# Performance work log

Hardware: AMD Instinct MI355X
Metric: run time of the kernel (lower is better)

Reference implementation:

```python
import math
import jax, jax.numpy as jnp
import numpy as np

B, S, H = 8, 1024, 1024
NH = 16
HD = H // NH  # 64


def setup_inputs() -> dict:
    key = jax.random.key(0)
    k1, k2, k3, k4 = jax.random.split(key, 4)
    hidden_states = jax.random.normal(k1, (B, S, H), dtype=jnp.float32)
    attention_mask = jax.random.randint(k2, (B, 1, 1, S), 0, 2, dtype=jnp.int32)
    w_qkv = jax.random.normal(k3, (H, 3 * H), dtype=jnp.float32) * (1.0 / math.sqrt(H))
    b_qkv = jax.random.normal(k4, (3 * H,), dtype=jnp.float32) * 0.02
    return {"hidden_states": hidden_states, "attention_mask": attention_mask,
            "w_qkv": w_qkv, "b_qkv": b_qkv}


def reference(hidden_states, attention_mask, w_qkv, b_qkv):
    b, s, _ = hidden_states.shape
    # fused QKV projection: [b, s, 3H]
    qkv = jnp.einsum('bsh,hk->bsk', hidden_states, w_qkv) + b_qkv
    # view (b, s, nh, 3*hd) -> permute -> chunk last dim (per-head q|k|v layout)
    qkv = qkv.reshape(b, s, NH, 3, HD)
    qkv = jnp.transpose(qkv, (0, 2, 1, 3, 4))      # [b, nh, s, 3, hd]
    q, k, v = qkv[..., 0, :], qkv[..., 1, :], qkv[..., 2, :]
    # raw scores, then FusedScaleMaskSoftmax semantics: scale * scores, mask, fp32 softmax
    scores = jnp.einsum('bhqd,bhkd->bhqk', q, k)
    scale = math.sqrt(HD)  # module passes sqrt(head_dim) as multiplicative scale
    scores = scores.astype(jnp.float32) * scale
    mask = attention_mask != 0                     # nonzero -> masked (padding)
    scores = jnp.where(mask, jnp.float32(-10000.0), scores)
    probs = jax.nn.softmax(scores, axis=-1).astype(hidden_states.dtype)
    # dropout prob = 0 -> identity
    context = jnp.einsum('bhqk,bhkd->bhqd', probs, v)
    context = jnp.transpose(context, (0, 2, 1, 3)).reshape(b, s, NH * HD)
    return context
```

## Files before the change

kernel.cpp:

```cpp
#include <hip/hip_runtime.h>
#include <math.h>

#define Bdim 8
#define Sdim 1024
#define Hdim 1024
#define NHd 16
#define HDd 64
#define N3H 3072

#define Q_OFF   0u
#define K_OFF   16777216u
#define V_OFF   33554432u
#define WH_OFF  41943040u
#define WL_OFF  45088768u
#define AHI_OFF 0u
#define ALO_OFF 8388608u

typedef __bf16 bf16x8 __attribute__((ext_vector_type(8)));
typedef float  f32x4  __attribute__((ext_vector_type(4)));

__device__ __forceinline__ unsigned short f2bf(float x) {
  unsigned b = __builtin_bit_cast(unsigned, x);
  return (unsigned short)((b + 0x7FFFu + ((b >> 16) & 1u)) >> 16);
}
__device__ __forceinline__ float bf2f(unsigned short h) {
  unsigned b = ((unsigned)h) << 16;
  return __builtin_bit_cast(float, b);
}
__device__ __forceinline__ void split_hl(float v, unsigned short& h, unsigned short& l) {
  h = f2bf(v);
  l = f2bf(v - bf2f(h));
}
__device__ __forceinline__ void async16(void* lds, const void* g) {
  __builtin_amdgcn_global_load_lds((const __attribute__((address_space(1))) unsigned int*)g,
                                   (__attribute__((address_space(3))) unsigned int*)lds, 16, 0, 0);
}

__global__ __launch_bounds__(256) void convert_A(
    const float* __restrict__ A, unsigned short* __restrict__ outp)
{
  size_t i = ((size_t)blockIdx.x * 256 + threadIdx.x) * 8;
  float4 a0 = *(const float4*)&A[i];
  float4 a1 = *(const float4*)&A[i + 4];
  float av[8] = {a0.x, a0.y, a0.z, a0.w, a1.x, a1.y, a1.z, a1.w};
  unsigned short h[8], l[8];
  #pragma unroll
  for (int j = 0; j < 8; ++j) split_hl(av[j], h[j], l[j]);
  *(uint4*)&outp[AHI_OFF + i] = *(uint4*)h;
  *(uint4*)&outp[ALO_OFF + i] = *(uint4*)l;
}

__global__ __launch_bounds__(256) void convert_W(
    const float* __restrict__ W, unsigned short* __restrict__ ws)
{
  __shared__ float T[64][65];
  const int tid = threadIdx.x;
  const int n0 = blockIdx.x * 64;
  const int k0 = blockIdx.y * 64;
  #pragma unroll
  for (int r = 0; r < 4; ++r) {
    int k = r * 16 + (tid >> 4);
    int n = (tid & 15) * 4;
    float4 v = *(const float4*)&W[(size_t)(k0 + k) * N3H + n0 + n];
    T[k][n + 0] = v.x; T[k][n + 1] = v.y; T[k][n + 2] = v.z; T[k][n + 3] = v.w;
  }
  __syncthreads();
  int n = tid >> 2;
  int kl = (tid & 3) * 16;
  unsigned short h[16], l[16];
  #pragma unroll
  for (int i = 0; i < 16; ++i) split_hl(T[kl + i][n], h[i], l[i]);
  size_t base = (size_t)(n0 + n) * 1024 + k0 + kl;
  *(uint4*)&ws[WH_OFF + base]     = *(uint4*)&h[0];
  *(uint4*)&ws[WH_OFF + base + 8] = *(uint4*)&h[8];
  *(uint4*)&ws[WL_OFF + base]     = *(uint4*)&l[0];
  *(uint4*)&ws[WL_OFF + base + 8] = *(uint4*)&l[8];
}

__global__ __launch_bounds__(256, 2) void qkv_mfma(
    const unsigned short* __restrict__ ao,
    const unsigned short* __restrict__ ws,
    const float* __restrict__ bias,
    unsigned short* __restrict__ wso)
{
  __shared__ unsigned short sA[2][128 * 32];
  __shared__ unsigned short sB[2][128 * 32];

  const int tid  = threadIdx.x;
  const int wave = tid >> 6;
  const int lane = tid & 63;
  const int l16  = lane & 15;
  const int quad = lane >> 4;

  const int n0 = blockIdx.x * 128;
  const int m0 = blockIdx.y * 128;
  const int wm = (wave >> 1) * 64;
  const int wn = (wave & 1) * 64;

  const unsigned short* Ah = ao + AHI_OFF;
  const unsigned short* Al = ao + ALO_OFF;
  const unsigned short* Wh = ws + WH_OFF;
  const unsigned short* Wl = ws + WL_OFF;

  f32x4 acc[4][4];
  #pragma unroll
  for (int i = 0; i < 4; ++i)
    #pragma unroll
    for (int j = 0; j < 4; ++j) acc[i][j] = (f32x4){0.f, 0.f, 0.f, 0.f};

  for (int kt = 0; kt < 1024; kt += 32) {
    __syncthreads();
    #pragma unroll
    for (int r = 0; r < 2; ++r) {
      int chunk = r * 256 + tid;
      int row = chunk >> 2;
      int c8  = (chunk & 3) << 3;
      int ldsoff = (r * 256 + wave * 64) * 8;
      async16(&sA[0][ldsoff], &Ah[(size_t)(m0 + row) * 1024 + kt + c8]);
      async16(&sA[1][ldsoff], &Al[(size_t)(m0 + row) * 1024 + kt + c8]);
      async16(&sB[0][ldsoff], &Wh[(size_t)(n0 + row) * 1024 + kt + c8]);
      async16(&sB[1][ldsoff], &Wl[(size_t)(n0 + row) * 1024 + kt + c8]);
    }
    __syncthreads();

    bf16x8 af[4][2], bf[4][2];
    #pragma unroll
    for (int i = 0; i < 4; ++i) {
      int row = wm + i * 16 + l16;
      af[i][0] = *(const bf16x8*)&sA[0][row * 32 + quad * 8];
      af[i][1] = *(const bf16x8*)&sA[1][row * 32 + quad * 8];
    }
    #pragma unroll
    for (int j = 0; j < 4; ++j) {
      int row = wn + j * 16 + l16;
      bf[j][0] = *(const bf16x8*)&sB[0][row * 32 + quad * 8];
      bf[j][1] = *(const bf16x8*)&sB[1][row * 32 + quad * 8];
    }
    #pragma unroll
    for (int i = 0; i < 4; ++i)
      #pragma unroll
      for (int j = 0; j < 4; ++j) {
        acc[i][j] = __builtin_amdgcn_mfma_f32_16x16x32_bf16(af[i][0], bf[j][0], acc[i][j], 0, 0, 0);
        acc[i][j] = __builtin_amdgcn_mfma_f32_16x16x32_bf16(af[i][1], bf[j][0], acc[i][j], 0, 0, 0);
        acc[i][j] = __builtin_amdgcn_mfma_f32_16x16x32_bf16(af[i][0], bf[j][1], acc[i][j], 0, 0, 0);
      }
  }

  const int ncol0 = n0 + wn;
  const int which = (ncol0 >> 6) % 3;
  const int head  = ncol0 / 192;
  const int mrow0 = m0 + wm;
  const int bb = mrow0 >> 10;
  const int sb = mrow0 & 1023;

  float bs[4];
  #pragma unroll
  for (int j = 0; j < 4; ++j) bs[j] = bias[ncol0 + j * 16 + l16];

  if (which < 2) {
    unsigned short* dst = wso + (which ? K_OFF : Q_OFF) +
        ((size_t)(bb * NHd + head) * Sdim + sb) * 128;
    #pragma unroll
    for (int i = 0; i < 4; ++i)
      #pragma unroll
      for (int j = 0; j < 4; ++j) {
        int d = j * 16 + l16;
        #pragma unroll
        for (int r = 0; r < 4; ++r) {
          int s = i * 16 + quad * 4 + r;
          float v = acc[i][j][r] + bs[j];
          unsigned short h, l;
          split_hl(v, h, l);
          dst[(size_t)s * 128 + d]      = h;
          dst[(size_t)s * 128 + 64 + d] = l;
        }
      }
  } else {
    unsigned short* dst = wso + V_OFF + (size_t)(bb * NHd + head) * HDd * Sdim;
    #pragma unroll
    for (int i = 0; i < 4; ++i)
      #pragma unroll
      for (int j = 0; j < 4; ++j) {
        int d = j * 16 + l16;
        int s0 = sb + i * 16 + quad * 4;
        unsigned short p[4];
        #pragma unroll
        for (int r = 0; r < 4; ++r) p[r] = f2bf(acc[i][j][r] + bs[j]);
        *(uint2*)&dst[(size_t)d * Sdim + s0] = *(uint2*)p;
      }
  }
}

__global__ __launch_bounds__(256, 2) void attn_mfma(
    const unsigned short* __restrict__ qhl,
    const unsigned short* __restrict__ khl,
    const unsigned short* __restrict__ vt,
    const int* __restrict__ mask,
    float* __restrict__ out)
{
  __shared__ unsigned short Ks[64][136];
  __shared__ unsigned short Vs[64][72];
  __shared__ unsigned short Pw[4][16][72];
  __shared__ float msk[64];

  const int tid  = threadIdx.x;
  const int wave = tid >> 6;
  const int lane = tid & 63;
  const int l16  = lane & 15;
  const int quad = lane >> 4;

  const int qt = blockIdx.x & 15;
  const int bh = blockIdx.x >> 4;
  const int bb = bh >> 4;
  const int q0 = qt * 64;

  {
    int row = tid >> 2, seg = tid & 3;
    const unsigned short* src = qhl + ((size_t)bh * Sdim + q0 + row) * 128;
    #pragma unroll
    for (int i = 0; i < 4; ++i) {
      int c = seg * 32 + i * 8;
      *(uint4*)&Ks[row][c] = *(const uint4*)&src[c];
    }
  }
  __syncthreads();
  bf16x8 qf[4];
  {
    int qrow = wave * 16 + l16;
    #pragma unroll
    for (int kk = 0; kk < 4; ++kk)
      qf[kk] = *(const bf16x8*)&Ks[qrow][kk * 32 + quad * 8];
  }

  f32x4 O[4] = {{0.f,0.f,0.f,0.f},{0.f,0.f,0.f,0.f},{0.f,0.f,0.f,0.f},{0.f,0.f,0.f,0.f}};
  float mrow[4] = {-INFINITY, -INFINITY, -INFINITY, -INFINITY};
  float lrow[4] = {0.f, 0.f, 0.f, 0.f};

  #pragma unroll 1
  for (int kt = 0; kt < Sdim / 64; ++kt) {
    __syncthreads();
    {
      int row = tid >> 2, seg = tid & 3;
      const unsigned short* src = khl + ((size_t)bh * Sdim + kt * 64 + row) * 128;
      #pragma unroll
      for (int i = 0; i < 4; ++i) {
        int c = seg * 32 + i * 8;
        *(uint4*)&Ks[row][c] = *(const uint4*)&src[c];
      }
    }
    {
      int d = tid >> 2, part = tid & 3;
      const unsigned short* src = vt + ((size_t)bh * HDd + d) * Sdim + kt * 64;
      *(uint4*)&Vs[d][part * 16]     = *(const uint4*)&src[part * 16];
      *(uint4*)&Vs[d][part * 16 + 8] = *(const uint4*)&src[part * 16 + 8];
    }
    if (tid < 64)
      msk[tid] = (mask[bb * Sdim + kt * 64 + tid] != 0) ? 1.f : 0.f;
    __syncthreads();

    f32x4 sc[4];
    #pragma unroll
    for (int ns = 0; ns < 4; ++ns) {
      f32x4 c = {0.f, 0.f, 0.f, 0.f};
      int krow = ns * 16 + l16;
      bf16x8 kf[4];
      #pragma unroll
      for (int kk = 0; kk < 4; ++kk)
        kf[kk] = *(const bf16x8*)&Ks[krow][kk * 32 + quad * 8];
      c = __builtin_amdgcn_mfma_f32_16x16x32_bf16(qf[0], kf[0], c, 0, 0, 0);
      c = __builtin_amdgcn_mfma_f32_16x16x32_bf16(qf[1], kf[1], c, 0, 0, 0);
      c = __builtin_amdgcn_mfma_f32_16x16x32_bf16(qf[2], kf[0], c, 0, 0, 0);
      c = __builtin_amdgcn_mfma_f32_16x16x32_bf16(qf[3], kf[1], c, 0, 0, 0);
      c = __builtin_amdgcn_mfma_f32_16x16x32_bf16(qf[0], kf[2], c, 0, 0, 0);
      c = __builtin_amdgcn_mfma_f32_16x16x32_bf16(qf[1], kf[3], c, 0, 0, 0);
      c = __builtin_amdgcn_mfma_f32_16x16x32_bf16(qf[2], kf[2], c, 0, 0, 0);
      c = __builtin_amdgcn_mfma_f32_16x16x32_bf16(qf[3], kf[3], c, 0, 0, 0);
      sc[ns] = c;
    }

    float rmax[4] = {-INFINITY, -INFINITY, -INFINITY, -INFINITY};
    #pragma unroll
    for (int ns = 0; ns < 4; ++ns) {
      float mk = msk[ns * 16 + l16];
      #pragma unroll
      for (int r = 0; r < 4; ++r) {
        float s = (mk != 0.f) ? -10000.f : sc[ns][r] * 8.f;
        sc[ns][r] = s;
        rmax[r] = fmaxf(rmax[r], s);
      }
    }
    #pragma unroll
    for (int r = 0; r < 4; ++r) {
      float v = rmax[r];
      v = fmaxf(v, __shfl_xor(v, 1, 16));
      v = fmaxf(v, __shfl_xor(v, 2, 16));
      v = fmaxf(v, __shfl_xor(v, 4, 16));
      v = fmaxf(v, __shfl_xor(v, 8, 16));
      rmax[r] = v;
    }

    float alpha[4];
    #pragma unroll
    for (int r = 0; r < 4; ++r) {
      float mn = fmaxf(mrow[r], rmax[r]);
      alpha[r] = __expf(mrow[r] - mn);
      mrow[r] = mn;
      lrow[r] *= alpha[r];
    }
    #pragma unroll
    for (int d = 0; d < 4; ++d)
      #pragma unroll
      for (int r = 0; r < 4; ++r) O[d][r] *= alpha[r];

    float rsum[4] = {0.f, 0.f, 0.f, 0.f};
    #pragma unroll
    for (int ns = 0; ns < 4; ++ns) {
      #pragma unroll
      for (int r = 0; r < 4; ++r) {
        float p = __expf(sc[ns][r] - mrow[r]);
        rsum[r] += p;
        Pw[wave][quad * 4 + r][ns * 16 + l16] = f2bf(p);
      }
    }
    #pragma unroll
    for (int r = 0; r < 4; ++r) {
      float v = rsum[r];
      v += __shfl_xor(v, 1, 16);
      v += __shfl_xor(v, 2, 16);
      v += __shfl_xor(v, 4, 16);
      v += __shfl_xor(v, 8, 16);
      lrow[r] += v;
    }

    bf16x8 pf[2];
    #pragma unroll
    for (int kk = 0; kk < 2; ++kk)
      pf[kk] = *(const bf16x8*)&Pw[wave][l16][kk * 32 + quad * 8];
    #pragma unroll
    for (int d = 0; d < 4; ++d) {
      int vrow = d * 16 + l16;
      #pragma unroll
      for (int kk = 0; kk < 2; ++kk) {
        bf16x8 vf = *(const bf16x8*)&Vs[vrow][kk * 32 + quad * 8];
        O[d] = __builtin_amdgcn_mfma_f32_16x16x32_bf16(pf[kk], vf, O[d], 0, 0, 0);
      }
    }
  }

  const int h = bh & 15;
  #pragma unroll
  for (int r = 0; r < 4; ++r) {
    float inv = 1.f / lrow[r];
    int q = q0 + wave * 16 + quad * 4 + r;
    float* dst = out + ((size_t)bb * Sdim + q) * Hdim + h * HDd;
    #pragma unroll
    for (int d = 0; d < 4; ++d)
      dst[d * 16 + l16] = O[d][r] * inv;
  }
}

extern "C" void kernel_launch(void* const* d_in, const int* in_sizes, int n_in,
                              void* d_out, int out_size, void* d_ws, size_t ws_size,
                              hipStream_t stream) {
  const float* hs   = (const float*)d_in[0];
  const int*   mask = (const int*)d_in[1];
  const float* w    = (const float*)d_in[2];
  const float* bias = (const float*)d_in[3];
  float* out = (float*)d_out;
  unsigned short* ws = (unsigned short*)d_ws;
  unsigned short* ao = (unsigned short*)d_out;

  convert_A<<<4096, 256, 0, stream>>>(hs, ao);
  convert_W<<<dim3(N3H / 64, 1024 / 64), 256, 0, stream>>>(w, ws);

  qkv_mfma<<<dim3(N3H / 128, 8192 / 128), 256, 0, stream>>>(ao, ws, bias, ws);

  attn_mfma<<<Bdim * NHd * (Sdim / 64), 256, 0, stream>>>(
      ws + Q_OFF, ws + K_OFF, ws + V_OFF, mask, out);
}
```

Measured before the change: 373.6 us.

## Process 128 queries per attention block and merge the input conversion kernels

The attention kernel now covers 128 query rows per block, two 16-row tiles per wave. Each K/V tile loaded into LDS is reused by twice as many queries, and the grid is reordered. Q fragments are loaded straight from global memory, and the whole mask row is preloaded into LDS once. The lo*lo term of the split-bf16 QK product is dropped, and the launch bound is raised to 4 blocks per SM. The two fp32-to-bf16 split kernels are merged into one launch. The trade-offs are more register pressure, fewer blocks in flight, and slightly lower score precision.

After: 869.4 us. 2.33x slower.

```diff
diff --git a/kernel.cpp b/kernel.cpp
--- a/kernel.cpp
+++ b/kernel.cpp
@@ -36,27 +36,28 @@
                                    (__attribute__((address_space(3))) unsigned int*)lds, 16, 0, 0);
 }
 
-__global__ __launch_bounds__(256) void convert_A(
-    const float* __restrict__ A, unsigned short* __restrict__ outp)
-{
-  size_t i = ((size_t)blockIdx.x * 256 + threadIdx.x) * 8;
-  float4 a0 = *(const float4*)&A[i];
-  float4 a1 = *(const float4*)&A[i + 4];
-  float av[8] = {a0.x, a0.y, a0.z, a0.w, a1.x, a1.y, a1.z, a1.w};
-  unsigned short h[8], l[8];
-  #pragma unroll
-  for (int j = 0; j < 8; ++j) split_hl(av[j], h[j], l[j]);
-  *(uint4*)&outp[AHI_OFF + i] = *(uint4*)h;
-  *(uint4*)&outp[ALO_OFF + i] = *(uint4*)l;
-}
-
-__global__ __launch_bounds__(256) void convert_W(
-    const float* __restrict__ W, unsigned short* __restrict__ ws)
+__global__ __launch_bounds__(256) void convert_AW(
+    const float* __restrict__ A, const float* __restrict__ W,
+    unsigned short* __restrict__ aout, unsigned short* __restrict__ ws)
 {
   __shared__ float T[64][65];
   const int tid = threadIdx.x;
-  const int n0 = blockIdx.x * 64;
-  const int k0 = blockIdx.y * 64;
+  int bid = blockIdx.x;
+  if (bid < 4096) {
+    size_t i = ((size_t)bid * 256 + tid) * 8;
+    float4 a0 = *(const float4*)&A[i];
+    float4 a1 = *(const float4*)&A[i + 4];
+    float av[8] = {a0.x, a0.y, a0.z, a0.w, a1.x, a1.y, a1.z, a1.w};
+    unsigned short h[8], l[8];
+    #pragma unroll
+    for (int j = 0; j < 8; ++j) split_hl(av[j], h[j], l[j]);
+    *(uint4*)&aout[AHI_OFF + i] = *(uint4*)h;
+    *(uint4*)&aout[ALO_OFF + i] = *(uint4*)l;
+    return;
+  }
+  bid -= 4096;
+  const int n0 = (bid % (N3H / 64)) * 64;
+  const int k0 = (bid / (N3H / 64)) * 64;
   #pragma unroll
   for (int r = 0; r < 4; ++r) {
     int k = r * 16 + (tid >> 4);
@@ -191,7 +192,7 @@
   }
 }
 
-__global__ __launch_bounds__(256, 2) void attn_mfma(
+__global__ __launch_bounds__(256, 4) void attn_mfma(
     const unsigned short* __restrict__ qhl,
     const unsigned short* __restrict__ khl,
     const unsigned short* __restrict__ vt,
@@ -201,7 +202,7 @@
   __shared__ unsigned short Ks[64][136];
   __shared__ unsigned short Vs[64][72];
   __shared__ unsigned short Pw[4][16][72];
-  __shared__ float msk[64];
+  __shared__ float msks[1024];
 
   const int tid  = threadIdx.x;
   const int wave = tid >> 6;
@@ -209,32 +210,39 @@
   const int l16  = lane & 15;
   const int quad = lane >> 4;
 
-  const int qt = blockIdx.x & 15;
-  const int bh = blockIdx.x >> 4;
+  const int bh = blockIdx.x & 127;
+  const int qt = blockIdx.x >> 7;
   const int bb = bh >> 4;
-  const int q0 = qt * 64;
+  const int q0 = qt * 128;
 
   {
-    int row = tid >> 2, seg = tid & 3;
-    const unsigned short* src = qhl + ((size_t)bh * Sdim + q0 + row) * 128;
-    #pragma unroll
-    for (int i = 0; i < 4; ++i) {
-      int c = seg * 32 + i * 8;
-      *(uint4*)&Ks[row][c] = *(const uint4*)&src[c];
-    }
-  }
-  __syncthreads();
-  bf16x8 qf[4];
-  {
-    int qrow = wave * 16 + l16;
+    int4 mv = *(const int4*)&mask[bb * Sdim + tid * 4];
+    msks[tid * 4 + 0] = mv.x ? 1.f : 0.f;
+    msks[tid * 4 + 1] = mv.y ? 1.f : 0.f;
+    msks[tid * 4 + 2] = mv.z ? 1.f : 0.f;
+    msks[tid * 4 + 3] = mv.w ? 1.f : 0.f;
+  }
+
+  bf16x8 qf[2][4];
+  #pragma unroll
+  for (int t = 0; t < 2; ++t) {
+    int row = q0 + wave * 32 + t * 16 + l16;
+    const unsigned short* src = qhl + ((size_t)bh * Sdim + row) * 128;
     #pragma unroll
     for (int kk = 0; kk < 4; ++kk)
-      qf[kk] = *(const bf16x8*)&Ks[qrow][kk * 32 + quad * 8];
-  }
-
-  f32x4 O[4] = {{0.f,0.f,0.f,0.f},{0.f,0.f,0.f,0.f},{0.f,0.f,0.f,0.f},{0.f,0.f,0.f,0.f}};
-  float mrow[4] = {-INFINITY, -INFINITY, -INFINITY, -INFINITY};
-  float lrow[4] = {0.f, 0.f, 0.f, 0.f};
+      qf[t][kk] = *(const bf16x8*)&src[kk * 32 + quad * 8];
+  }
+
+  f32x4 O[2][4];
+  float mrow[2][4], lrow[2][4];
+  #pragma unroll
+  for (int t = 0; t < 2; ++t)
+    #pragma unroll
+    for (int d = 0; d < 4; ++d) {
+      O[t][d] = (f32x4){0.f, 0.f, 0.f, 0.f};
+      mrow[t][d] = -INFINITY;
+      lrow[t][d] = 0.f;
+    }
 
   #pragma unroll 1
   for (int kt = 0; kt < Sdim / 64; ++kt) {
@@ -254,109 +262,110 @@
       *(uint4*)&Vs[d][part * 16]     = *(const uint4*)&src[part * 16];
       *(uint4*)&Vs[d][part * 16 + 8] = *(const uint4*)&src[part * 16 + 8];
     }
-    if (tid < 64)
-      msk[tid] = (mask[bb * Sdim + kt * 64 + tid] != 0) ? 1.f : 0.f;
     __syncthreads();
 
-    f32x4 sc[4];
-    #pragma unroll
-    for (int ns = 0; ns < 4; ++ns) {
-      f32x4 c = {0.f, 0.f, 0.f, 0.f};
-      int krow = ns * 16 + l16;
-      bf16x8 kf[4];
-      #pragma unroll
-      for (int kk = 0; kk < 4; ++kk)
-        kf[kk] = *(const bf16x8*)&Ks[krow][kk * 32 + quad * 8];
-      c = __builtin_amdgcn_mfma_f32_16x16x32_bf16(qf[0], kf[0], c, 0, 0, 0);
-      c = __builtin_amdgcn_mfma_f32_16x16x32_bf16(qf[1], kf[1], c, 0, 0, 0);
-      c = __builtin_amdgcn_mfma_f32_16x16x32_bf16(qf[2], kf[0], c, 0, 0, 0);
-      c = __builtin_amdgcn_mfma_f32_16x16x32_bf16(qf[3], kf[1], c, 0, 0, 0);
-      c = __builtin_amdgcn_mfma_f32_16x16x32_bf16(qf[0], kf[2], c, 0, 0, 0);
-      c = __builtin_amdgcn_mfma_f32_16x16x32_bf16(qf[1], kf[3], c, 0, 0, 0);
-      c = __builtin_amdgcn_mfma_f32_16x16x32_bf16(qf[2], kf[2], c, 0, 0, 0);
-      c = __builtin_amdgcn_mfma_f32_16x16x32_bf16(qf[3], kf[3], c, 0, 0, 0);
-      sc[ns] = c;
-    }
-
-    float rmax[4] = {-INFINITY, -INFINITY, -INFINITY, -INFINITY};
-    #pragma unroll
-    for (int ns = 0; ns < 4; ++ns) {
-      float mk = msk[ns * 16 + l16];
+    #pragma unroll 1
+    for (int t = 0; t < 2; ++t) {
+      f32x4 sc[4];
+      #pragma unroll
+      for (int ns = 0; ns < 4; ++ns) {
+        f32x4 c = {0.f, 0.f, 0.f, 0.f};
+        int krow = ns * 16 + l16;
+        bf16x8 kf[4];
+        #pragma unroll
+        for (int kk = 0; kk < 4; ++kk)
+          kf[kk] = *(const bf16x8*)&Ks[krow][kk * 32 + quad * 8];
+        c = __builtin_amdgcn_mfma_f32_16x16x32_bf16(qf[t][0], kf[0], c, 0, 0, 0);
+        c = __builtin_amdgcn_mfma_f32_16x16x32_bf16(qf[t][1], kf[1], c, 0, 0, 0);
+        c = __builtin_amdgcn_mfma_f32_16x16x32_bf16(qf[t][2], kf[0], c, 0, 0, 0);
+        c = __builtin_amdgcn_mfma_f32_16x16x32_bf16(qf[t][3], kf[1], c, 0, 0, 0);
+        c = __builtin_amdgcn_mfma_f32_16x16x32_bf16(qf[t][0], kf[2], c, 0, 0, 0);
+        c = __builtin_amdgcn_mfma_f32_16x16x32_bf16(qf[t][1], kf[3], c, 0, 0, 0);
+        sc[ns] = c;
+      }
+
+      float rmax[4] = {-INFINITY, -INFINITY, -INFINITY, -INFINITY};
+      #pragma unroll
+      for (int ns = 0; ns < 4; ++ns) {
+        float mk = msks[kt * 64 + ns * 16 + l16];
+        #pragma unroll
+        for (int r = 0; r < 4; ++r) {
+          float s = (mk != 0.f) ? -10000.f : sc[ns][r] * 8.f;
+          sc[ns][r] = s;
+          rmax[r] = fmaxf(rmax[r], s);
+        }
+      }
       #pragma unroll
       for (int r = 0; r < 4; ++r) {
-        float s = (mk != 0.f) ? -10000.f : sc[ns][r] * 8.f;
-        sc[ns][r] = s;
-        rmax[r] = fmaxf(rmax[r], s);
-      }
-    }
+        float v = rmax[r];
+        v = fmaxf(v, __shfl_xor(v, 1, 16));
+        v = fmaxf(v, __shfl_xor(v, 2, 16));
+        v = fmaxf(v, __shfl_xor(v, 4, 16));
+        v = fmaxf(v, __shfl_xor(v, 8, 16));
+        rmax[r] = v;
+      }
+
+      float alpha[4];
+      #pragma unroll
+      for (int r = 0; r < 4; ++r) {
+        float mn = fmaxf(mrow[t][r], rmax[r]);
+        alpha[r] = __expf(mrow[t][r] - mn);
+        mrow[t][r] = mn;
+        lrow[t][r] *= alpha[r];
+      }
+      #pragma unroll
+      for (int d = 0; d < 4; ++d)
+        #pragma unroll
+        for (int r = 0; r < 4; ++r) O[t][d][r] *= alpha[r];
+
+      float rsum[4] = {0.f, 0.f, 0.f, 0.f};
+      #pragma unroll
+      for (int ns = 0; ns < 4; ++ns) {
+        #pragma unroll
+        for (int r = 0; r < 4; ++r) {
+          float p = __expf(sc[ns][r] - mrow[t][r]);
+          rsum[r] += p;
+          Pw[wave][quad * 4 + r][ns * 16 + l16] = f2bf(p);
+        }
+      }
+      #pragma unroll
+      for (int r = 0; r < 4; ++r) {
+        float v = rsum[r];
+        v += __shfl_xor(v, 1, 16);
+        v += __shfl_xor(v, 2, 16);
+        v += __shfl_xor(v, 4, 16);
+        v += __shfl_xor(v, 8, 16);
+        lrow[t][r] += v;
+      }
+
+      bf16x8 pf[2];
+      #pragma unroll
+      for (int kk = 0; kk < 2; ++kk)
+        pf[kk] = *(const bf16x8*)&Pw[wave][l16][kk * 32 + quad * 8];
+      #pragma unroll
+      for (int d = 0; d < 4; ++d) {
+        int vrow = d * 16 + l16;
+        #pragma unroll
+        for (int kk = 0; kk < 2; ++kk) {
+          bf16x8 vf = *(const bf16x8*)&Vs[vrow][kk * 32 + quad * 8];
+          O[t][d] = __builtin_amdgcn_mfma_f32_16x16x32_bf16(pf[kk], vf, O[t][d], 0, 0, 0);
+        }
+      }
+    }
+  }
+
+  const int h = bh & 15;
+  #pragma unroll
+  for (int t = 0; t < 2; ++t)
     #pragma unroll
     for (int r = 0; r < 4; ++r) {
-      float v = rmax[r];
-      v = fmaxf(v, __shfl_xor(v, 1, 16));
-      v = fmaxf(v, __shfl_xor(v, 2, 16));
-      v = fmaxf(v, __shfl_xor(v, 4, 16));
-      v = fmaxf(v, __shfl_xor(v, 8, 16));
-      rmax[r] = v;
-    }
-
-    float alpha[4];
-    #pragma unroll
-    for (int r = 0; r < 4; ++r) {
-      float mn = fmaxf(mrow[r], rmax[r]);
-      alpha[r] = __expf(mrow[r] - mn);
-      mrow[r] = mn;
-      lrow[r] *= alpha[r];
-    }
-    #pragma unroll
-    for (int d = 0; d < 4; ++d)
-      #pragma unroll
-      for (int r = 0; r < 4; ++r) O[d][r] *= alpha[r];
-
-    float rsum[4] = {0.f, 0.f, 0.f, 0.f};
-    #pragma unroll
-    for (int ns = 0; ns < 4; ++ns) {
-      #pragma unroll
-      for (int r = 0; r < 4; ++r) {
-        float p = __expf(sc[ns][r] - mrow[r]);
-        rsum[r] += p;
-        Pw[wave][quad * 4 + r][ns * 16 + l16] = f2bf(p);
-      }
-    }
-    #pragma unroll
-    for (int r = 0; r < 4; ++r) {
-      float v = rsum[r];
-      v += __shfl_xor(v, 1, 16);
-      v += __shfl_xor(v, 2, 16);
-      v += __shfl_xor(v, 4, 16);
-      v += __shfl_xor(v, 8, 16);
-      lrow[r] += v;
-    }
-
-    bf16x8 pf[2];
-    #pragma unroll
-    for (int kk = 0; kk < 2; ++kk)
-      pf[kk] = *(const bf16x8*)&Pw[wave][l16][kk * 32 + quad * 8];
-    #pragma unroll
-    for (int d = 0; d < 4; ++d) {
-      int vrow = d * 16 + l16;
-      #pragma unroll
-      for (int kk = 0; kk < 2; ++kk) {
-        bf16x8 vf = *(const bf16x8*)&Vs[vrow][kk * 32 + quad * 8];
-        O[d] = __builtin_amdgcn_mfma_f32_16x16x32_bf16(pf[kk], vf, O[d], 0, 0, 0);
-      }
-    }
-  }
-
-  const int h = bh & 15;
-  #pragma unroll
-  for (int r = 0; r < 4; ++r) {
-    float inv = 1.f / lrow[r];
-    int q = q0 + wave * 16 + quad * 4 + r;
-    float* dst = out + ((size_t)bb * Sdim + q) * Hdim + h * HDd;
-    #pragma unroll
-    for (int d = 0; d < 4; ++d)
-      dst[d * 16 + l16] = O[d][r] * inv;
-  }
+      float inv = 1.f / lrow[t][r];
+      int q = q0 + wave * 32 + t * 16 + quad * 4 + r;
+      float* dst = out + ((size_t)bb * Sdim + q) * Hdim + h * HDd;
+      #pragma unroll
+      for (int d = 0; d < 4; ++d)
+        dst[d * 16 + l16] = O[t][d][r] * inv;
+    }
 }
 
 extern "C" void kernel_launch(void* const* d_in, const int* in_sizes, int n_in,
@@ -370,11 +379,10 @@
   unsigned short* ws = (unsigned short*)d_ws;
   unsigned short* ao = (unsigned short*)d_out;
 
-  convert_A<<<4096, 256, 0, stream>>>(hs, ao);
-  convert_W<<<dim3(N3H / 64, 1024 / 64), 256, 0, stream>>>(w, ws);
+  convert_AW<<<4096 + (N3H / 64) * (1024 / 64), 256, 0, stream>>>(hs, w, ao, ws);
 
   qkv_mfma<<<dim3(N3H / 128, 8192 / 128), 256, 0, stream>>>(ao, ws, bias, ws);
 
-  attn_mfma<<<Bdim * NHd * (Sdim / 64), 256, 0, stream>>>(
+  attn_mfma<<<Bdim * NHd * (Sdim / 128), 256, 0, stream>>>(
       ws + Q_OFF, ws + K_OFF, ws + V_OFF, mask, out);
 }
```
